# Kernel tuning notes

Measured on AMD Instinct MI355X. Metric: run time of the kernel, lower is better.

## Reference

```python
import jax, jax.numpy as jnp
import numpy as np

D = 512
H = 4 * D
EPS = 1e-5

def layernorm(x, g, b):
    mu = jnp.mean(x, axis=-1, keepdims=True)
    var = jnp.mean((x - mu) ** 2, axis=-1, keepdims=True)
    return (x - mu) * jax.lax.rsqrt(var + EPS) * g + b

def setup_inputs() -> dict:
    key = jax.random.key(0)
    ks = jax.random.split(key, 16)
    s = 0.02
    inp = {
        "x": jax.random.normal(ks[0], (16, 2048, D), dtype=jnp.float32),
        "wq": jax.random.normal(ks[1], (D, D), dtype=jnp.float32) * s,
        "bq": jnp.zeros((D,), jnp.float32),
        "wk": jax.random.normal(ks[2], (D, D), dtype=jnp.float32) * s,
        "bk": jnp.zeros((D,), jnp.float32),
        "wv": jax.random.normal(ks[3], (D, D), dtype=jnp.float32) * s,
        "bv": jnp.zeros((D,), jnp.float32),
        "wp": jax.random.normal(ks[4], (D, D), dtype=jnp.float32) * s,
        "bp": jnp.zeros((D,), jnp.float32),
        "w1": jax.random.normal(ks[5], (D, H), dtype=jnp.float32) * s,
        "b1": jnp.zeros((H,), jnp.float32),
        "w2": jax.random.normal(ks[6], (H, D), dtype=jnp.float32) * s,
        "b2": jnp.zeros((D,), jnp.float32),
        "g1": jnp.ones((D,), jnp.float32),
        "be1": jnp.zeros((D,), jnp.float32),
        "g2": jnp.ones((D,), jnp.float32),
        "be2": jnp.zeros((D,), jnp.float32),
    }
    return inp

def reference(x, wq, bq, wk, bk, wv, bv, wp, bp, w1, b1, w2, b2, g1, be1, g2, be2):
    temperature = jnp.sqrt(jnp.asarray(D, x.dtype))
    q = x @ wq + bq                      # [B,N,D]
    k = x @ wk + bk
    v = x @ wv + bv
    energy = jnp.einsum('bnd,bmd->bnm', q / temperature, k)   # [B,N,N]
    attn = jax.nn.softmax(energy, axis=-1)
    out = jnp.einsum('bnm,bmd->bnd', attn, v)
    att = out @ wp + bp
    x = layernorm(x + att, g1, be1)
    h = jax.nn.gelu(x @ w1 + b1, approximate=False)
    ff = h @ w2 + b2
    x = layernorm(x + ff, g2, be2)
    return x
```

## Files before the change

### kernel.cpp

```cpp
#include <hip/hip_runtime.h>
#include <cmath>

typedef __bf16 bf16_t;
typedef __bf16 bf16x8 __attribute__((ext_vector_type(8)));
typedef __bf16 bf16x4 __attribute__((ext_vector_type(4)));
typedef float f32x4 __attribute__((ext_vector_type(4)));

#define DEV_INLINE __device__ __forceinline__

DEV_INLINE void gload_lds16(const void* g, void* l) {
  __builtin_amdgcn_global_load_lds(
      (const __attribute__((address_space(1))) void*)g,
      (__attribute__((address_space(3))) void*)l, 16, 0, 0);
}

DEV_INLINE float gelu_f(float v) {
  const float u = v * (0.7978845608f + 0.0356774081f * v * v);
  const float e = __expf(2.f * u);
  const float th = 1.f - 2.f / (e + 1.f);
  return 0.5f * v * (1.f + th);
}

template<int EPI, bool HAS_BIAS>
__global__ __launch_bounds__(256, 2)
void gemm_bt(const bf16_t* __restrict__ A, const bf16_t* __restrict__ B,
             const float* __restrict__ bias, void* __restrict__ C,
             bf16_t* __restrict__ vTaux,
             int M, int N, int K, int lda, int ldb, int ldc,
             long sA, long sB, long sC, float scale)
{
  __shared__ alignas(16) bf16_t lds[3][2][4096];
  const int b = blockIdx.z;
  A += (long)b * sA;
  B += (long)b * sB;
  const int t  = threadIdx.x;
  const int l  = t & 63;
  const int w  = t >> 6;
  const int wr = (w >> 1) * 64;
  const int wc = (w & 1) * 64;

  const int gx  = gridDim.x;
  const int nwg = gx * gridDim.y;
  int id = blockIdx.y * gx + blockIdx.x;
  id = (id & 7) * (nwg >> 3) + (id >> 3);
  const int m0 = (id / gx) * 128;
  const int n0 = (id % gx) * 128;

  const int r0 = t >> 2;
  const int r1 = r0 + 64;
  const int wb = (t & 3) * 16;
  const int cb0 = wb ^ (((r0 >> 1) & 3) << 4);
  const int cb1 = wb ^ (((r1 >> 1) & 3) << 4);
  const bf16_t* gA0 = A + (long)(m0 + r0) * lda + (cb0 >> 1);
  const bf16_t* gA1 = A + (long)(m0 + r1) * lda + (cb1 >> 1);
  const bf16_t* gB0 = B + (long)(n0 + r0) * ldb + (cb0 >> 1);
  const bf16_t* gB1 = B + (long)(n0 + r1) * ldb + (cb1 >> 1);

#define STAGE(kt, q) do {                                   \
    const long kofs_ = (long)(kt) * 32;                     \
    gload_lds16(gA0 + kofs_, &lds[q][0][t * 8]);            \
    gload_lds16(gA1 + kofs_, &lds[q][0][2048 + t * 8]);     \
    gload_lds16(gB0 + kofs_, &lds[q][1][t * 8]);            \
    gload_lds16(gB1 + kofs_, &lds[q][1][2048 + t * 8]);     \
  } while (0)

  const int fr  = l & 15;
  const int kkb = (l >> 4) * 16;
  int offA[4], offB[4];
#pragma unroll
  for (int mi = 0; mi < 4; mi++) {
    const int row = wr + mi * 16 + fr;
    offA[mi] = row * 32 + ((kkb ^ (((row >> 1) & 3) << 4)) >> 1);
  }
#pragma unroll
  for (int ni = 0; ni < 4; ni++) {
    const int row = wc + ni * 16 + fr;
    offB[ni] = row * 32 + ((kkb ^ (((row >> 1) & 3) << 4)) >> 1);
  }

  f32x4 acc[4][4] = {};

  const int NT = K >> 5;
  STAGE(0, 0);
  STAGE(1, 1);

  int q = 0;
  for (int kt = 0; kt < NT; ++kt) {
    if (kt < NT - 1) asm volatile("s_waitcnt vmcnt(4)" ::: "memory");
    else             asm volatile("s_waitcnt vmcnt(0)" ::: "memory");
    __builtin_amdgcn_sched_barrier(0);
    __builtin_amdgcn_s_barrier();

    if (kt + 2 < NT) {
      int qs = q + 2; if (qs >= 3) qs -= 3;
      STAGE(kt + 2, qs);
    }

    bf16x8 af[4], bfr[4];
#pragma unroll
    for (int mi = 0; mi < 4; mi++)
      af[mi] = *(const bf16x8*)&lds[q][0][offA[mi]];
#pragma unroll
    for (int ni = 0; ni < 4; ni++)
      bfr[ni] = *(const bf16x8*)&lds[q][1][offB[ni]];
#pragma unroll
    for (int mi = 0; mi < 4; mi++)
#pragma unroll
      for (int ni = 0; ni < 4; ni++)
        acc[mi][ni] = __builtin_amdgcn_mfma_f32_16x16x32_bf16(
            af[mi], bfr[ni], acc[mi][ni], 0, 0, 0);

    if (++q == 3) q = 0;
  }
#undef STAGE

  const long cb = (long)b * sC;
  const int rbase = m0 + wr + (l >> 4) * 4;
#pragma unroll
  for (int mi = 0; mi < 4; mi++) {
    const int row0 = rbase + mi * 16;
#pragma unroll
    for (int ni = 0; ni < 4; ni++) {
      const int c = n0 + wc + ni * 16 + fr;
      float bias_v = 0.f;
      if constexpr (HAS_BIAS) bias_v = bias[c];
      float vals[4];
#pragma unroll
      for (int r = 0; r < 4; r++) {
        float v = acc[mi][ni][r] + bias_v;
        if constexpr (EPI == 2) v *= scale;
        if constexpr (EPI == 3) v = gelu_f(v);
        vals[r] = v;
      }
      if constexpr (EPI == 5) {
        if (c < 1024) {
#pragma unroll
          for (int r = 0; r < 4; r++)
            ((bf16_t*)C)[(long)(row0 + r) * ldc + c] = (bf16_t)vals[r];
        } else {
          const int bb = row0 >> 11;
          const int n  = row0 & 2047;
          bf16x4 pk = { (bf16_t)vals[0], (bf16_t)vals[1],
                        (bf16_t)vals[2], (bf16_t)vals[3] };
          *(bf16x4*)&vTaux[(long)bb * (512 * 2048) + (long)(c - 1024) * 2048 + n] = pk;
        }
      } else {
#pragma unroll
        for (int r = 0; r < 4; r++) {
          const long idx = cb + (long)(row0 + r) * ldc + c;
          if constexpr (EPI == 0) ((float*)C)[idx] = vals[r];
          else                    ((bf16_t*)C)[idx] = (bf16_t)vals[r];
        }
      }
    }
  }
}

__global__ __launch_bounds__(256)
void transpose_cast(const float* __restrict__ in, bf16_t* __restrict__ out,
                    int R, int Cc)
{
  __shared__ float tile[32][33];
  const int c0 = blockIdx.x * 32;
  const int r0 = blockIdx.y * 32;
  const int tx = threadIdx.x & 31;
  const int ty = threadIdx.x >> 5;
#pragma unroll
  for (int i = 0; i < 32; i += 8)
    tile[ty + i][tx] = in[(long)(r0 + ty + i) * Cc + (c0 + tx)];
  __syncthreads();
#pragma unroll
  for (int i = 0; i < 32; i += 8)
    out[(long)(c0 + ty + i) * R + (r0 + tx)] = (bf16_t)tile[tx][ty + i];
}

__global__ __launch_bounds__(256)
void cast_to_bf16(const float* __restrict__ in, bf16_t* __restrict__ out, long n)
{
  const long i = ((long)blockIdx.x * 256 + threadIdx.x) * 4;
  if (i >= n) return;
  const float4 v = *(const float4*)&in[i];
  bf16x4 o = { (bf16_t)v.x, (bf16_t)v.y, (bf16_t)v.z, (bf16_t)v.w };
  *(bf16x4*)&out[i] = o;
}

__global__ __launch_bounds__(256)
void concat_bias(const float* __restrict__ a, const float* __restrict__ b,
                 const float* __restrict__ c, float* __restrict__ o)
{
  const int i = blockIdx.x * 256 + threadIdx.x;
  if (i < 512) o[i] = a[i];
  else if (i < 1024) o[i] = b[i - 512];
  else if (i < 1536) o[i] = c[i - 1024];
}

__global__ __launch_bounds__(256)
void softmax2048(bf16_t* __restrict__ E)
{
  const long row = blockIdx.x;
  bf16_t* p = E + row * 2048;
  const int t = threadIdx.x;
  bf16x8 xv = *(const bf16x8*)&p[t * 8];
  float v[8];
#pragma unroll
  for (int j = 0; j < 8; j++) v[j] = (float)xv[j];
  float m = v[0];
#pragma unroll
  for (int j = 1; j < 8; j++) m = fmaxf(m, v[j]);
  for (int o = 32; o; o >>= 1) m = fmaxf(m, __shfl_xor(m, o));
  __shared__ float redm[4];
  __shared__ float reds[4];
  if ((t & 63) == 0) redm[t >> 6] = m;
  __syncthreads();
  m = fmaxf(fmaxf(redm[0], redm[1]), fmaxf(redm[2], redm[3]));
  float s = 0.f;
#pragma unroll
  for (int j = 0; j < 8; j++) { v[j] = __expf(v[j] - m); s += v[j]; }
  for (int o = 32; o; o >>= 1) s += __shfl_xor(s, o);
  if ((t & 63) == 0) reds[t >> 6] = s;
  __syncthreads();
  s = reds[0] + reds[1] + reds[2] + reds[3];
  const float inv = 1.f / s;
  bf16x8 ov;
#pragma unroll
  for (int j = 0; j < 8; j++) ov[j] = (bf16_t)(v[j] * inv);
  *(bf16x8*)&p[t * 8] = ov;
}

template<bool A_BF16, bool EMIT_F32, bool EMIT_BF16>
__global__ __launch_bounds__(128)
void add_ln(const void* __restrict__ xa_, const float* __restrict__ xadd,
            const float* __restrict__ g, const float* __restrict__ be,
            float* __restrict__ y, bf16_t* __restrict__ yb)
{
  const long row = blockIdx.x;
  const int c = threadIdx.x * 4;
  float av[4];
  if constexpr (A_BF16) {
    const bf16_t* xa = (const bf16_t*)xa_;
    bf16x4 a = *(const bf16x4*)&xa[row * 512 + c];
#pragma unroll
    for (int j = 0; j < 4; j++) av[j] = (float)a[j];
  } else {
    const float* xa = (const float*)xa_;
    const float4 a = *(const float4*)&xa[row * 512 + c];
    av[0] = a.x; av[1] = a.y; av[2] = a.z; av[3] = a.w;
  }
  const float4 bb = *(const float4*)&xadd[row * 512 + c];
  float vv[4] = { av[0] + bb.x, av[1] + bb.y, av[2] + bb.z, av[3] + bb.w };
  float s = 0.f, s2 = 0.f;
#pragma unroll
  for (int j = 0; j < 4; j++) { s += vv[j]; s2 += vv[j] * vv[j]; }
  for (int o = 32; o; o >>= 1) { s += __shfl_xor(s, o); s2 += __shfl_xor(s2, o); }
  __shared__ float r0[2], r1[2];
  const int w = threadIdx.x >> 6;
  if ((threadIdx.x & 63) == 0) { r0[w] = s; r1[w] = s2; }
  __syncthreads();
  s = r0[0] + r0[1]; s2 = r1[0] + r1[1];
  const float mu = s * (1.f / 512.f);
  const float var = s2 * (1.f / 512.f) - mu * mu;
  const float rstd = rsqrtf(var + 1e-5f);
  const float4 gg = *(const float4*)&g[c];
  const float4 bev = *(const float4*)&be[c];
  float o0 = (vv[0] - mu) * rstd * gg.x + bev.x;
  float o1 = (vv[1] - mu) * rstd * gg.y + bev.y;
  float o2 = (vv[2] - mu) * rstd * gg.z + bev.z;
  float o3 = (vv[3] - mu) * rstd * gg.w + bev.w;
  if constexpr (EMIT_F32) {
    float4 yo = { o0, o1, o2, o3 };
    *(float4*)&y[row * 512 + c] = yo;
  }
  if constexpr (EMIT_BF16) {
    bf16x4 ob = { (bf16_t)o0, (bf16_t)o1, (bf16_t)o2, (bf16_t)o3 };
    *(bf16x4*)&yb[row * 512 + c] = ob;
  }
}

extern "C" void kernel_launch(void* const* d_in, const int* in_sizes, int n_in,
                              void* d_out, int out_size, void* d_ws, size_t ws_size,
                              hipStream_t stream)
{
  const float* x   = (const float*)d_in[0];
  const float* wq  = (const float*)d_in[1];
  const float* bq  = (const float*)d_in[2];
  const float* wk  = (const float*)d_in[3];
  const float* bk  = (const float*)d_in[4];
  const float* wv  = (const float*)d_in[5];
  const float* bv  = (const float*)d_in[6];
  const float* wp  = (const float*)d_in[7];
  const float* bp  = (const float*)d_in[8];
  const float* w1  = (const float*)d_in[9];
  const float* b1  = (const float*)d_in[10];
  const float* w2  = (const float*)d_in[11];
  const float* b2  = (const float*)d_in[12];
  const float* g1  = (const float*)d_in[13];
  const float* be1 = (const float*)d_in[14];
  const float* g2  = (const float*)d_in[15];
  const float* be2 = (const float*)d_in[16];

  const long S = 16L * 2048 * 512;
  const long Mi = 1L << 20;

  const size_t NEED = (size_t)200 * Mi;
  if (ws_size < NEED) return;

  char* wsp = (char*)d_ws;
  bf16_t* wqkvT = (bf16_t*)(wsp + 0);
  bf16_t* wpT   = wqkvT + 1536L * 512;
  bf16_t* w1T   = wpT + 512L * 512;
  bf16_t* w2T   = w1T + 2048L * 512;
  float*  bqkv  = (float*)(w2T + 512L * 2048);
  bf16_t* xb  = (bf16_t*)(wsp +   8 * Mi);
  bf16_t* qkb = (bf16_t*)(wsp +  40 * Mi);
  bf16_t* vT  = (bf16_t*)(wsp + 104 * Mi);
  bf16_t* E   = (bf16_t*)(wsp + 136 * Mi);
  bf16_t* ob  = xb;
  bf16_t* x1b = qkb;
  bf16_t* h   = (bf16_t*)(wsp + 72 * Mi);

  cast_to_bf16<<<dim3((unsigned)(S / 4 / 256)), 256, 0, stream>>>(x, xb, S);

  transpose_cast<<<dim3(16, 16), 256, 0, stream>>>(wq, wqkvT,               512, 512);
  transpose_cast<<<dim3(16, 16), 256, 0, stream>>>(wk, wqkvT + 512L * 512,  512, 512);
  transpose_cast<<<dim3(16, 16), 256, 0, stream>>>(wv, wqkvT + 1024L * 512, 512, 512);
  transpose_cast<<<dim3(16, 16), 256, 0, stream>>>(wp, wpT, 512, 512);
  transpose_cast<<<dim3(64, 16), 256, 0, stream>>>(w1, w1T, 512, 2048);
  transpose_cast<<<dim3(16, 64), 256, 0, stream>>>(w2, w2T, 2048, 512);
  concat_bias<<<dim3(6), 256, 0, stream>>>(bq, bk, bv, bqkv);

  gemm_bt<5, true><<<dim3(12, 256, 1), 256, 0, stream>>>(
      xb, wqkvT, bqkv, qkb, vT, 32768, 1536, 512, 512, 512, 1024, 0, 0, 0, 0.f);

  for (int cgrp = 0; cgrp < 2; cgrp++) {
    const long qoff = (long)cgrp * 8 * 2048 * 1024;
    gemm_bt<2, false><<<dim3(16, 16, 8), 256, 0, stream>>>(
        qkb + qoff, qkb + qoff + 512, nullptr, E, nullptr,
        2048, 2048, 512, 1024, 1024, 2048,
        2048L * 1024, 2048L * 1024, 2048L * 2048, 0.04419417382f);
    softmax2048<<<dim3(16384), 256, 0, stream>>>(E);
    gemm_bt<1, false><<<dim3(4, 16, 8), 256, 0, stream>>>(
        E, vT + (long)cgrp * 8 * 512 * 2048, nullptr,
        ob + (long)cgrp * 8 * 2048 * 512, nullptr,
        2048, 512, 2048, 2048, 2048, 512,
        2048L * 2048, 512L * 2048, 2048L * 512, 0.f);
  }

  gemm_bt<0, true><<<dim3(4, 256, 1), 256, 0, stream>>>(
      ob, wpT, bp, (float*)d_out, nullptr,
      32768, 512, 512, 512, 512, 512, 0, 0, 0, 0.f);

  add_ln<false, false, true><<<dim3(32768), 128, 0, stream>>>(
      x, (float*)d_out, g1, be1, nullptr, x1b);

  gemm_bt<3, true><<<dim3(16, 256, 1), 256, 0, stream>>>(
      x1b, w1T, b1, h, nullptr, 32768, 2048, 512, 512, 512, 2048, 0, 0, 0, 0.f);

  gemm_bt<0, true><<<dim3(4, 256, 1), 256, 0, stream>>>(
      h, w2T, b2, (float*)d_out, nullptr,
      32768, 512, 2048, 2048, 2048, 512, 0, 0, 0, 0.f);

  add_ln<true, true, false><<<dim3(32768), 128, 0, stream>>>(
      x1b, (float*)d_out, g2, be2, (float*)d_out, nullptr);
}
```

Before: 622.6 us.

## Stage bf16 GEMM epilogues through LDS and keep projection/FFN outputs in bf16

Adds an LDS-staged epilogue for bf16-output GEMMs. Tiles are written to a swizzled shared buffer and then stored as coalesced 16-byte rows, replacing scattered 2-byte stores. The attention projection and FFN2 GEMMs now emit bf16 into workspace instead of fp32 into the output. The residual add+layernorm reads bf16 for both operands, including the bf16 copy of x instead of fp32 x. This cuts global traffic and store inefficiency, at the cost of extra precision loss in the residual path and a larger workspace.

After: 654.9 us. 1.05x slower.

```diff
diff --git a/kernel.cpp b/kernel.cpp
--- a/kernel.cpp
+++ b/kernel.cpp
@@ -49,12 +49,12 @@
   const int r0 = t >> 2;
   const int r1 = r0 + 64;
   const int wb = (t & 3) * 16;
-  const int cb0 = wb ^ (((r0 >> 1) & 3) << 4);
-  const int cb1 = wb ^ (((r1 >> 1) & 3) << 4);
-  const bf16_t* gA0 = A + (long)(m0 + r0) * lda + (cb0 >> 1);
-  const bf16_t* gA1 = A + (long)(m0 + r1) * lda + (cb1 >> 1);
-  const bf16_t* gB0 = B + (long)(n0 + r0) * ldb + (cb0 >> 1);
-  const bf16_t* gB1 = B + (long)(n0 + r1) * ldb + (cb1 >> 1);
+  const int cbs0 = wb ^ (((r0 >> 1) & 3) << 4);
+  const int cbs1 = wb ^ (((r1 >> 1) & 3) << 4);
+  const bf16_t* gA0 = A + (long)(m0 + r0) * lda + (cbs0 >> 1);
+  const bf16_t* gA1 = A + (long)(m0 + r1) * lda + (cbs1 >> 1);
+  const bf16_t* gB0 = B + (long)(n0 + r0) * ldb + (cbs0 >> 1);
+  const bf16_t* gB1 = B + (long)(n0 + r1) * ldb + (cbs1 >> 1);
 
 #define STAGE(kt, q) do {                                   \
     const long kofs_ = (long)(kt) * 32;                     \
@@ -115,6 +115,41 @@
 #undef STAGE
 
   const long cb = (long)b * sC;
+
+  if constexpr (EPI == 1 || EPI == 2 || EPI == 3) {
+    bf16_t* ct = &lds[0][0][0];
+    __syncthreads();
+    const int lr = wr + (l >> 4) * 4;
+#pragma unroll
+    for (int mi = 0; mi < 4; mi++) {
+#pragma unroll
+      for (int ni = 0; ni < 4; ni++) {
+        const int cl = wc + ni * 16 + fr;
+        float bias_v = 0.f;
+        if constexpr (HAS_BIAS) bias_v = bias[n0 + cl];
+#pragma unroll
+        for (int r = 0; r < 4; r++) {
+          const int row = lr + mi * 16 + r;
+          float v = acc[mi][ni][r] + bias_v;
+          if constexpr (EPI == 2) v *= scale;
+          if constexpr (EPI == 3) v = gelu_f(v);
+          ct[row * 128 + (((cl * 2) ^ ((row & 7) << 4)) >> 1)] = (bf16_t)v;
+        }
+      }
+    }
+    __syncthreads();
+    const int orow = t >> 1;
+    const int obyt = (t & 1) * 128;
+    bf16_t* cout = (bf16_t*)C + cb + (long)(m0 + orow) * ldc + n0 + (obyt >> 1);
+#pragma unroll
+    for (int i = 0; i < 8; i++) {
+      const int byte = (obyt + i * 16) ^ ((orow & 7) << 4);
+      bf16x8 v8 = *(const bf16x8*)&ct[orow * 128 + (byte >> 1)];
+      *(bf16x8*)(cout + i * 8) = v8;
+    }
+    return;
+  }
+
   const int rbase = m0 + wr + (l >> 4) * 4;
 #pragma unroll
   for (int mi = 0; mi < 4; mi++) {
@@ -126,12 +161,7 @@
       if constexpr (HAS_BIAS) bias_v = bias[c];
       float vals[4];
 #pragma unroll
-      for (int r = 0; r < 4; r++) {
-        float v = acc[mi][ni][r] + bias_v;
-        if constexpr (EPI == 2) v *= scale;
-        if constexpr (EPI == 3) v = gelu_f(v);
-        vals[r] = v;
-      }
+      for (int r = 0; r < 4; r++) vals[r] = acc[mi][ni][r] + bias_v;
       if constexpr (EPI == 5) {
         if (c < 1024) {
 #pragma unroll
@@ -146,11 +176,8 @@
         }
       } else {
 #pragma unroll
-        for (int r = 0; r < 4; r++) {
-          const long idx = cb + (long)(row0 + r) * ldc + c;
-          if constexpr (EPI == 0) ((float*)C)[idx] = vals[r];
-          else                    ((bf16_t*)C)[idx] = (bf16_t)vals[r];
-        }
+        for (int r = 0; r < 4; r++)
+          ((float*)C)[cb + (long)(row0 + r) * ldc + c] = vals[r];
       }
     }
   }
@@ -227,27 +254,19 @@
   *(bf16x8*)&p[t * 8] = ov;
 }
 
-template<bool A_BF16, bool EMIT_F32, bool EMIT_BF16>
+template<bool EMIT_F32, bool EMIT_BF16>
 __global__ __launch_bounds__(128)
-void add_ln(const void* __restrict__ xa_, const float* __restrict__ xadd,
+void add_ln(const bf16_t* __restrict__ xa, const bf16_t* __restrict__ xadd,
             const float* __restrict__ g, const float* __restrict__ be,
             float* __restrict__ y, bf16_t* __restrict__ yb)
 {
   const long row = blockIdx.x;
   const int c = threadIdx.x * 4;
-  float av[4];
-  if constexpr (A_BF16) {
-    const bf16_t* xa = (const bf16_t*)xa_;
-    bf16x4 a = *(const bf16x4*)&xa[row * 512 + c];
-#pragma unroll
-    for (int j = 0; j < 4; j++) av[j] = (float)a[j];
-  } else {
-    const float* xa = (const float*)xa_;
-    const float4 a = *(const float4*)&xa[row * 512 + c];
-    av[0] = a.x; av[1] = a.y; av[2] = a.z; av[3] = a.w;
-  }
-  const float4 bb = *(const float4*)&xadd[row * 512 + c];
-  float vv[4] = { av[0] + bb.x, av[1] + bb.y, av[2] + bb.z, av[3] + bb.w };
+  bf16x4 a = *(const bf16x4*)&xa[row * 512 + c];
+  bf16x4 d = *(const bf16x4*)&xadd[row * 512 + c];
+  float vv[4];
+#pragma unroll
+  for (int j = 0; j < 4; j++) vv[j] = (float)a[j] + (float)d[j];
   float s = 0.f, s2 = 0.f;
 #pragma unroll
   for (int j = 0; j < 4; j++) { s += vv[j]; s2 += vv[j] * vv[j]; }
@@ -301,7 +320,7 @@
   const long S = 16L * 2048 * 512;
   const long Mi = 1L << 20;
 
-  const size_t NEED = (size_t)200 * Mi;
+  const size_t NEED = (size_t)232 * Mi;
   if (ws_size < NEED) return;
 
   char* wsp = (char*)d_ws;
@@ -310,13 +329,15 @@
   bf16_t* w1T   = wpT + 512L * 512;
   bf16_t* w2T   = w1T + 2048L * 512;
   float*  bqkv  = (float*)(w2T + 512L * 2048);
-  bf16_t* xb  = (bf16_t*)(wsp +   8 * Mi);
-  bf16_t* qkb = (bf16_t*)(wsp +  40 * Mi);
-  bf16_t* vT  = (bf16_t*)(wsp + 104 * Mi);
-  bf16_t* E   = (bf16_t*)(wsp + 136 * Mi);
-  bf16_t* ob  = xb;
-  bf16_t* x1b = qkb;
-  bf16_t* h   = (bf16_t*)(wsp + 72 * Mi);
+  bf16_t* xb    = (bf16_t*)(wsp +   8 * Mi);
+  bf16_t* qkb   = (bf16_t*)(wsp +  40 * Mi);
+  bf16_t* vT    = (bf16_t*)(wsp + 104 * Mi);
+  bf16_t* E     = (bf16_t*)(wsp + 136 * Mi);
+  bf16_t* ob    = (bf16_t*)(wsp + 200 * Mi);
+  bf16_t* x1b   = qkb;
+  bf16_t* h     = (bf16_t*)(wsp + 72 * Mi);
+  bf16_t* projb = E;
+  bf16_t* ffb   = xb;
 
   cast_to_bf16<<<dim3((unsigned)(S / 4 / 256)), 256, 0, stream>>>(x, xb, S);
 
@@ -345,20 +366,20 @@
         2048L * 2048, 512L * 2048, 2048L * 512, 0.f);
   }
 
-  gemm_bt<0, true><<<dim3(4, 256, 1), 256, 0, stream>>>(
-      ob, wpT, bp, (float*)d_out, nullptr,
+  gemm_bt<1, true><<<dim3(4, 256, 1), 256, 0, stream>>>(
+      ob, wpT, bp, projb, nullptr,
       32768, 512, 512, 512, 512, 512, 0, 0, 0, 0.f);
 
-  add_ln<false, false, true><<<dim3(32768), 128, 0, stream>>>(
-      x, (float*)d_out, g1, be1, nullptr, x1b);
+  add_ln<false, true><<<dim3(32768), 128, 0, stream>>>(
+      xb, projb, g1, be1, nullptr, x1b);
 
   gemm_bt<3, true><<<dim3(16, 256, 1), 256, 0, stream>>>(
       x1b, w1T, b1, h, nullptr, 32768, 2048, 512, 512, 512, 2048, 0, 0, 0, 0.f);
 
-  gemm_bt<0, true><<<dim3(4, 256, 1), 256, 0, stream>>>(
-      h, w2T, b2, (float*)d_out, nullptr,
+  gemm_bt<1, true><<<dim3(4, 256, 1), 256, 0, stream>>>(
+      h, w2T, b2, ffb, nullptr,
       32768, 512, 2048, 2048, 2048, 512, 0, 0, 0, 0.f);
 
-  add_ln<true, true, false><<<dim3(32768), 128, 0, stream>>>(
-      x1b, (float*)d_out, g2, be2, (float*)d_out, nullptr);
-}
+  add_ln<true, false><<<dim3(32768), 128, 0, stream>>>(
+      x1b, ffb, g2, be2, (float*)d_out, nullptr);
+}
```
